# Kernel tuning notes

Hardware: AMD Instinct MI355X
Metric: run time of the kernel (lower is better)

Reference implementation:

```python
import jax, jax.numpy as jnp
import numpy as np

B, CIN, H, W = 1024, 1, 200, 32   # batch, in_channels, feat_nums, embed_dim
COUT = 16                          # out_channels
K = 3                              # con_kernel (height)
TOPK = 50                          # min(feat_nums, topk)
# ZeroPad2d padding for kernel (K,1): width (0,0), height (K//2 + K - 2*(K//2) - 1, K//2)
PAD_TOP = K // 2 + K - 2 * (K // 2) - 1
PAD_BOT = K // 2


def setup_inputs() -> dict:
    key = jax.random.key(0)
    k1, k2, k3 = jax.random.split(key, 3)
    x = jax.random.normal(k1, (B, CIN, H, W), dtype=jnp.float32)
    conv_w = jax.random.normal(k2, (COUT, CIN, K, 1), dtype=jnp.float32) * 0.1
    conv_b = jax.random.normal(k3, (COUT,), dtype=jnp.float32) * 0.1
    return {"x": x, "conv_w": conv_w, "conv_b": conv_b}


def reference(x, conv_w, conv_b):
    # 'same' conv along H only (kernel width is 1), stride 1
    y = jax.lax.conv_general_dilated(
        x, conv_w,
        window_strides=(1, 1),
        padding=((PAD_TOP, PAD_BOT), (0, 0)),
        dimension_numbers=("NCHW", "OIHW", "NCHW"),
    )
    y = jnp.tanh(y + conv_b[None, :, None, None])  # [B, COUT, H, W]
    # top-k along H (dim 2), values sorted descending (matches torch.topk)
    yt = jnp.swapaxes(y, 2, 3)                      # [B, COUT, W, H]
    vals, _ = jax.lax.top_k(yt, TOPK)               # [B, COUT, W, TOPK]
    return jnp.swapaxes(vals, 2, 3)                 # [B, COUT, TOPK, W]
```

## Files before the change

### kernel.cpp

```cpp
#include <hip/hip_runtime.h>
#include <math.h>

#define B_     1024
#define H_     200
#define W_     32
#define COUT_  16
#define TOPK_  50

#define XST 17
#define OST 17

typedef _Float16 h2 __attribute__((ext_vector_type(2)));
union HU { h2 h; int i; };

constexpr unsigned long long lane_mask(int J, int K) {
    unsigned long long m = 0;
    for (int l = 0; l < 64; ++l) {
        bool a = (l & J) != 0;
        bool b = (K < 64) && ((l & K) != 0);
        if (a != b) m |= (1ull << l);
    }
    return m;
}

#define X_1(o,v)  "v_mov_b32_dpp " o ", " v " quad_perm:[1,0,3,2] row_mask:0xf bank_mask:0xf\n\t"
#define X_2(o,v)  "v_mov_b32_dpp " o ", " v " quad_perm:[2,3,0,1] row_mask:0xf bank_mask:0xf\n\t"
#define X_8(o,v)  "v_mov_b32_dpp " o ", " v " row_ror:8 row_mask:0xf bank_mask:0xf\n\t"
#define X_4(o,v)  "ds_swizzle_b32 " o ", " v " offset:0x101F\n\t"
#define X_16(o,v) "ds_swizzle_b32 " o ", " v " offset:0x401F\n\t"
#define X_32(o,v) "ds_bpermute_b32 " o ", %[pa], " v "\n\t"
#define PRE_1  "s_nop 4\n\t"
#define PRE_2  "s_nop 4\n\t"
#define PRE_8  "s_nop 4\n\t"
#define PRE_4  ""
#define PRE_16 ""
#define PRE_32 ""
#define WAIT_1  ""
#define WAIT_2  ""
#define WAIT_8  ""
#define WAIT_4  "s_waitcnt lgkmcnt(0)\n\t"
#define WAIT_16 "s_waitcnt lgkmcnt(0)\n\t"
#define WAIT_32 "s_waitcnt lgkmcnt(0)\n\t"

#define S6(J, K) { constexpr unsigned long long M = lane_mask(J, K); \
  int o0,o1,o2,o3,o4,o5; \
  asm volatile( PRE_##J \
    X_##J("%[o0]","%[x0]") X_##J("%[o1]","%[x1]") X_##J("%[o2]","%[x2]") \
    X_##J("%[o3]","%[x3]") X_##J("%[o4]","%[x4]") X_##J("%[o5]","%[x5]") \
    WAIT_##J \
    "s_mov_b64 exec, %[m]\n\t" \
    "v_pk_max_f16 %[x0], %[x0], %[o0]\n\t" \
    "v_pk_max_f16 %[x1], %[x1], %[o1]\n\t" \
    "v_pk_min_f16 %[x2], %[x2], %[o2]\n\t" \
    "v_pk_min_f16 %[x3], %[x3], %[o3]\n\t" \
    "v_pk_max_f16 %[x4], %[x4], %[o4]\n\t" \
    "v_pk_max_f16 %[x5], %[x5], %[o5]\n\t" \
    "s_not_b64 exec, exec\n\t" \
    "v_pk_min_f16 %[x0], %[x0], %[o0]\n\t" \
    "v_pk_min_f16 %[x1], %[x1], %[o1]\n\t" \
    "v_pk_max_f16 %[x2], %[x2], %[o2]\n\t" \
    "v_pk_max_f16 %[x3], %[x3], %[o3]\n\t" \
    "v_pk_min_f16 %[x4], %[x4], %[o4]\n\t" \
    "v_pk_min_f16 %[x5], %[x5], %[o5]\n\t" \
    "s_mov_b64 exec, -1\n\t" \
    : [x0]"+v"(v0a),[x1]"+v"(v0b),[x2]"+v"(v1a),[x3]"+v"(v1b),[x4]"+v"(v2a),[x5]"+v"(v2b), \
      [o0]"=&v"(o0),[o1]"=&v"(o1),[o2]"=&v"(o2),[o3]"=&v"(o3),[o4]"=&v"(o4),[o5]"=&v"(o5) \
    : [m]"s"(M), [pa]"v"(paddr)); }

#define P2N(J, K, A, B) { constexpr unsigned long long M = lane_mask(J, K); \
  int oA,oB; \
  asm volatile( PRE_##J \
    X_##J("%[xA2]","%[xA]") X_##J("%[xB2]","%[xB]") \
    WAIT_##J \
    "s_mov_b64 exec, %[m]\n\t" \
    "v_pk_min_f16 %[xA], %[xA], %[xA2]\n\t" \
    "v_pk_min_f16 %[xB], %[xB], %[xB2]\n\t" \
    "s_not_b64 exec, exec\n\t" \
    "v_pk_max_f16 %[xA], %[xA], %[xA2]\n\t" \
    "v_pk_max_f16 %[xB], %[xB], %[xB2]\n\t" \
    "s_mov_b64 exec, -1\n\t" \
    : [xA]"+v"(A),[xB]"+v"(B),[xA2]"=&v"(oA),[xB2]"=&v"(oB) \
    : [m]"s"(M), [pa]"v"(paddr)); }

#define M4(J) { constexpr unsigned long long M = lane_mask(J, 64); \
  int o0,o1,o2,o3; \
  asm volatile( PRE_##J \
    X_##J("%[o0]","%[x0]") X_##J("%[o1]","%[x1]") X_##J("%[o2]","%[x2]") X_##J("%[o3]","%[x3]") \
    WAIT_##J \
    "s_mov_b64 exec, %[m]\n\t" \
    "v_pk_max_f16 %[x0], %[x0], %[o0]\n\t" \
    "v_pk_max_f16 %[x1], %[x1], %[o1]\n\t" \
    "v_pk_min_f16 %[x2], %[x2], %[o2]\n\t" \
    "v_pk_min_f16 %[x3], %[x3], %[o3]\n\t" \
    "s_not_b64 exec, exec\n\t" \
    "v_pk_min_f16 %[x0], %[x0], %[o0]\n\t" \
    "v_pk_min_f16 %[x1], %[x1], %[o1]\n\t" \
    "v_pk_max_f16 %[x2], %[x2], %[o2]\n\t" \
    "v_pk_max_f16 %[x3], %[x3], %[o3]\n\t" \
    "s_mov_b64 exec, -1\n\t" \
    : [x0]"+v"(m1a),[x1]"+v"(m1b),[x2]"+v"(m2a),[x3]"+v"(m2b), \
      [o0]"=&v"(o0),[o1]"=&v"(o1),[o2]"=&v"(o2),[o3]"=&v"(o3) \
    : [m]"s"(M), [pa]"v"(paddr)); }

__device__ __forceinline__ int pkmax(int a, int b) {
    int r;
    asm("v_pk_max_f16 %0, %1, %2" : "=v"(r) : "v"(a), "v"(b));
    return r;
}

__device__ __forceinline__ float fast_tanh(float s) {
    float e = __expf(2.0f * s);
    return fmaf(-2.0f, __builtin_amdgcn_rcpf(e + 1.0f), 1.0f);
}

__global__ __launch_bounds__(256, 8) void cnn_topk_kernel(
    const float* __restrict__ x,
    const float* __restrict__ cw,
    const float* __restrict__ cb,
    float* __restrict__ out)
{
    __shared__ float xs[(H_ + 2) * XST];
    __shared__ int   obuf[TOPK_ * OST];

    const int b   = blockIdx.x >> 1;
    const int wh  = blockIdx.x & 1;
    const int tid = threadIdx.x;
    const float* xb = x + (size_t)b * (H_ * W_) + wh * 16;

    for (int i = tid; i < H_ * 4; i += 256) {
        int h = i >> 2, q = (i & 3) * 4;
        float4 v = *reinterpret_cast<const float4*>(xb + h * W_ + q);
        float* d = &xs[(h + 1) * XST + q];
        d[0] = v.x; d[1] = v.y; d[2] = v.z; d[3] = v.w;
    }
    if (tid < 16) {
        xs[tid] = 0.0f;
        xs[(H_ + 1) * XST + tid] = 0.0f;
    }
    __syncthreads();

    const int wave = tid >> 6;
    const int lane = tid & 63;
    const int paddr = (lane ^ 32) << 2;

    const int SENT = (int)0xFC00FC00;
    const int h3 = (192 + lane < H_) ? (192 + lane) : (H_ - 1);

#pragma unroll 1
    for (int cp = 0; cp < 8; ++cp) {
        const int coA = 2 * cp, coB = 2 * cp + 1;
        const float w0A = cw[coA * 3], w1A = cw[coA * 3 + 1], w2A = cw[coA * 3 + 2], bA = cb[coA];
        const float w0B = cw[coB * 3], w1B = cw[coB * 3 + 1], w2B = cw[coB * 3 + 2], bB = cb[coB];

#pragma unroll
        for (int wp = 0; wp < 2; ++wp) {
            const int wA = wave * 4 + wp * 2;
            const int wB = wA + 1;

            int v0a, v1a, v2a, v3a, v0b, v1b, v2b, v3b;
#define MAKE_V(VR, HROW, WC)                                                 \
            {   const int hh = (HROW);                                       \
                float xm = xs[ hh      * XST + (WC)];                        \
                float xc = xs[(hh + 1) * XST + (WC)];                        \
                float xp = xs[(hh + 2) * XST + (WC)];                        \
                float sA = fmaf(w2A, xp, fmaf(w1A, xc, fmaf(w0A, xm, bA)));  \
                float sB = fmaf(w2B, xp, fmaf(w1B, xc, fmaf(w0B, xm, bB)));  \
                VR = __builtin_bit_cast(int, __builtin_amdgcn_cvt_pkrtz(sA, sB)); }
            MAKE_V(v0a, lane, wA)       MAKE_V(v0b, lane, wB)
            MAKE_V(v1a, 64 + lane, wA)  MAKE_V(v1b, 64 + lane, wB)
            MAKE_V(v2a, 128 + lane, wA) MAKE_V(v2b, 128 + lane, wB)
            MAKE_V(v3a, h3, wA)         MAKE_V(v3b, h3, wB)
#undef MAKE_V
            v3a = (lane < 8) ? v3a : SENT;
            v3b = (lane < 8) ? v3b : SENT;

            S6(1, 2)
            S6(2, 4)  S6(1, 4)
            S6(4, 8)  S6(2, 8)  S6(1, 8)
            S6(8, 16) S6(4, 16) S6(2, 16) S6(1, 16)
            S6(16,32) S6(8, 32) S6(4, 32) S6(2, 32) S6(1, 32)
            S6(32,64) S6(16,64) S6(8, 64) S6(4, 64) S6(2, 64) S6(1, 64)

            P2N(1, 2, v3a, v3b)
            P2N(2, 4, v3a, v3b)  P2N(1, 4, v3a, v3b)
            P2N(4, 8, v3a, v3b)  P2N(2, 8, v3a, v3b)  P2N(1, 8, v3a, v3b)

            int m1a = pkmax(v0a, v1a), m1b = pkmax(v0b, v1b);
            int m2a = pkmax(v2a, v3a), m2b = pkmax(v2b, v3b);
            M4(32) M4(16) M4(8) M4(4) M4(2) M4(1)
            int ta = pkmax(m1a, m2a), tb = pkmax(m1b, m2b);
            P2N(32, 64, ta, tb) P2N(16, 64, ta, tb) P2N(8, 64, ta, tb)
            P2N(4, 64, ta, tb)  P2N(2, 64, ta, tb)  P2N(1, 64, ta, tb)

            if (lane < TOPK_) {
                obuf[lane * OST + wA] = ta;
                obuf[lane * OST + wB] = tb;
            }
        }
        __syncthreads();

#pragma unroll
        for (int j = 0; j < 4; ++j) {
            int idx = tid + j * 256;
            if (idx < 800) {
                int k = idx >> 4, w2 = idx & 15;
                HU u; u.i = obuf[k * OST + w2];
                size_t o0 = (((size_t)b * COUT_ + coA) * TOPK_ + k) * W_ + wh * 16 + w2;
                out[o0]                        = fast_tanh((float)u.h.x);
                out[o0 + (size_t)TOPK_ * W_]   = fast_tanh((float)u.h.y);
            }
        }
        __syncthreads();
    }
}

extern "C" void kernel_launch(void* const* d_in, const int* in_sizes, int n_in,
                              void* d_out, int out_size, void* d_ws, size_t ws_size,
                              hipStream_t stream) {
    const float* x  = (const float*)d_in[0];
    const float* cw = (const float*)d_in[1];
    const float* cb = (const float*)d_in[2];
    float* out = (float*)d_out;

    cnn_topk_kernel<<<dim3(B_ * 2), dim3(256), 0, stream>>>(x, cw, cb, out);
}
```

Baseline: 250.5 us.

## Restructure bitonic top-k so each 16-lane group handles one column

Each 16-lane group now owns one output column and holds 13 packed half2 values per lane, where before a full wave sorted 200 rows of one column pair. Most bitonic stages become in-register compare-exchanges, and lane exchanges only use DPP and ds_swizzle within 16 lanes, so the ds_bpermute and xor-16 swizzle are gone. This removes cross-row LDS permute traffic and the serial loop over column pairs per wave. The cost is more live registers and a more intricate merge network, with some risk to correctness.

Measured after the change: 230.0 us. 8.2% less time.

```diff
diff --git a/kernel.cpp b/kernel.cpp
--- a/kernel.cpp
+++ b/kernel.cpp
@@ -13,100 +13,146 @@
 typedef _Float16 h2 __attribute__((ext_vector_type(2)));
 union HU { h2 h; int i; };
 
-constexpr unsigned long long lane_mask(int J, int K) {
+
+constexpr unsigned long long lmask(int d, int Kb) {
     unsigned long long m = 0;
     for (int l = 0; l < 64; ++l) {
-        bool a = (l & J) != 0;
-        bool b = (K < 64) && ((l & K) != 0);
+        int ln = l & 15;
+        bool a = (ln & d) != 0;
+        bool b = Kb && ((ln & Kb) != 0);
         if (a != b) m |= (1ull << l);
     }
     return m;
 }
 
-#define X_1(o,v)  "v_mov_b32_dpp " o ", " v " quad_perm:[1,0,3,2] row_mask:0xf bank_mask:0xf\n\t"
-#define X_2(o,v)  "v_mov_b32_dpp " o ", " v " quad_perm:[2,3,0,1] row_mask:0xf bank_mask:0xf\n\t"
-#define X_8(o,v)  "v_mov_b32_dpp " o ", " v " row_ror:8 row_mask:0xf bank_mask:0xf\n\t"
-#define X_4(o,v)  "ds_swizzle_b32 " o ", " v " offset:0x101F\n\t"
-#define X_16(o,v) "ds_swizzle_b32 " o ", " v " offset:0x401F\n\t"
-#define X_32(o,v) "ds_bpermute_b32 " o ", %[pa], " v "\n\t"
-#define PRE_1  "s_nop 4\n\t"
-#define PRE_2  "s_nop 4\n\t"
-#define PRE_8  "s_nop 4\n\t"
-#define PRE_4  ""
-#define PRE_16 ""
-#define PRE_32 ""
-#define WAIT_1  ""
-#define WAIT_2  ""
-#define WAIT_8  ""
-#define WAIT_4  "s_waitcnt lgkmcnt(0)\n\t"
-#define WAIT_16 "s_waitcnt lgkmcnt(0)\n\t"
-#define WAIT_32 "s_waitcnt lgkmcnt(0)\n\t"
-
-#define S6(J, K) { constexpr unsigned long long M = lane_mask(J, K); \
-  int o0,o1,o2,o3,o4,o5; \
-  asm volatile( PRE_##J \
-    X_##J("%[o0]","%[x0]") X_##J("%[o1]","%[x1]") X_##J("%[o2]","%[x2]") \
-    X_##J("%[o3]","%[x3]") X_##J("%[o4]","%[x4]") X_##J("%[o5]","%[x5]") \
-    WAIT_##J \
+#define XOP_1(o,v) "v_mov_b32_dpp " o ", " v " quad_perm:[1,0,3,2] row_mask:0xf bank_mask:0xf\n\t"
+#define XOP_2(o,v) "v_mov_b32_dpp " o ", " v " quad_perm:[2,3,0,1] row_mask:0xf bank_mask:0xf\n\t"
+#define XOP_8(o,v) "v_mov_b32_dpp " o ", " v " row_ror:8 row_mask:0xf bank_mask:0xf\n\t"
+#define XOP_4(o,v) "ds_swizzle_b32 " o ", " v " offset:0x101F\n\t"
+#define PRE_1 "s_nop 4\n\t"
+#define PRE_2 "s_nop 4\n\t"
+#define PRE_8 "s_nop 4\n\t"
+#define PRE_4 ""
+#define WAIT_1 ""
+#define WAIT_2 ""
+#define WAIT_8 ""
+#define WAIT_4 "s_waitcnt lgkmcnt(0)\n\t"
+
+#define P1_MX "v_pk_max_f16 "
+#define P1_MN "v_pk_min_f16 "
+#define P2_MX "v_pk_min_f16 "
+#define P2_MN "v_pk_max_f16 "
+#define OP_(ph,t,x,o) ph##_##t x ", " x ", " o "\n\t"
+
+#define SRT12(d, Kb, t0,t1,t2,t3,t4,t5,t6,t7,t8,t9,tA,tB) { \
+  constexpr unsigned long long M_ = lmask(d, Kb); \
+  int o0,o1,o2,o3,o4,o5,o6,o7,o8,o9,oA,oB; \
+  asm volatile( PRE_##d \
+    XOP_##d("%[o0]","%[x0]") XOP_##d("%[o1]","%[x1]") \
+    XOP_##d("%[o2]","%[x2]") XOP_##d("%[o3]","%[x3]") \
+    XOP_##d("%[o4]","%[x4]") XOP_##d("%[o5]","%[x5]") \
+    XOP_##d("%[o6]","%[x6]") XOP_##d("%[o7]","%[x7]") \
+    XOP_##d("%[o8]","%[x8]") XOP_##d("%[o9]","%[x9]") \
+    XOP_##d("%[oA]","%[xA]") XOP_##d("%[oB]","%[xB]") \
+    WAIT_##d \
+    "s_mov_b64 exec, %[m]\n\t" \
+    OP_(P1,t0,"%[x0]","%[o0]") OP_(P1,t1,"%[x1]","%[o1]") \
+    OP_(P1,t2,"%[x2]","%[o2]") OP_(P1,t3,"%[x3]","%[o3]") \
+    OP_(P1,t4,"%[x4]","%[o4]") OP_(P1,t5,"%[x5]","%[o5]") \
+    OP_(P1,t6,"%[x6]","%[o6]") OP_(P1,t7,"%[x7]","%[o7]") \
+    OP_(P1,t8,"%[x8]","%[o8]") OP_(P1,t9,"%[x9]","%[o9]") \
+    OP_(P1,tA,"%[xA]","%[oA]") OP_(P1,tB,"%[xB]","%[oB]") \
+    "s_not_b64 exec, exec\n\t" \
+    OP_(P2,t0,"%[x0]","%[o0]") OP_(P2,t1,"%[x1]","%[o1]") \
+    OP_(P2,t2,"%[x2]","%[o2]") OP_(P2,t3,"%[x3]","%[o3]") \
+    OP_(P2,t4,"%[x4]","%[o4]") OP_(P2,t5,"%[x5]","%[o5]") \
+    OP_(P2,t6,"%[x6]","%[o6]") OP_(P2,t7,"%[x7]","%[o7]") \
+    OP_(P2,t8,"%[x8]","%[o8]") OP_(P2,t9,"%[x9]","%[o9]") \
+    OP_(P2,tA,"%[xA]","%[oA]") OP_(P2,tB,"%[xB]","%[oB]") \
+    "s_mov_b64 exec, -1\n\t" \
+    : [x0]"+v"(a0),[x1]"+v"(a1),[x2]"+v"(a2),[x3]"+v"(a3), \
+      [x4]"+v"(b0),[x5]"+v"(b1),[x6]"+v"(b2),[x7]"+v"(b3), \
+      [x8]"+v"(e0),[x9]"+v"(e1),[xA]"+v"(e2),[xB]"+v"(e3), \
+      [o0]"=&v"(o0),[o1]"=&v"(o1),[o2]"=&v"(o2),[o3]"=&v"(o3), \
+      [o4]"=&v"(o4),[o5]"=&v"(o5),[o6]"=&v"(o6),[o7]"=&v"(o7), \
+      [o8]"=&v"(o8),[o9]"=&v"(o9),[oA]"=&v"(oA),[oB]"=&v"(oB) \
+    : [m]"s"(M_)); }
+
+#define SRT_A(d,Kb) SRT12(d,Kb, MX,MX,MX,MX, MN,MN,MN,MN, MX,MX,MX,MX)
+#define SRT_B(d)    SRT12(d,0,  MX,MN,MX,MN, MN,MX,MN,MX, MX,MN,MX,MN)
+#define SRT_C(d)    SRT12(d,0,  MX,MX,MN,MN, MN,MN,MX,MX, MX,MX,MN,MN)
+
+#define C3(d, Kb) { constexpr unsigned long long M_ = lmask(d, Kb); int oF; \
+  asm volatile( PRE_##d XOP_##d("%[oF]","%[xF]") WAIT_##d \
+    "s_mov_b64 exec, %[m]\n\t" \
+    "v_pk_min_f16 %[xF], %[xF], %[oF]\n\t" \
+    "s_not_b64 exec, exec\n\t" \
+    "v_pk_max_f16 %[xF], %[xF], %[oF]\n\t" \
+    "s_mov_b64 exec, -1\n\t" \
+    : [xF]"+v"(f0), [oF]"=&v"(oF) : [m]"s"(M_)); }
+
+#define MRG8(d) { constexpr unsigned long long M_ = lmask(d, 0); \
+  int o0,o1,o2,o3,o4,o5,o6,o7; \
+  asm volatile( PRE_##d \
+    XOP_##d("%[o0]","%[x0]") XOP_##d("%[o1]","%[x1]") \
+    XOP_##d("%[o2]","%[x2]") XOP_##d("%[o3]","%[x3]") \
+    XOP_##d("%[o4]","%[x4]") XOP_##d("%[o5]","%[x5]") \
+    XOP_##d("%[o6]","%[x6]") XOP_##d("%[o7]","%[x7]") \
+    WAIT_##d \
     "s_mov_b64 exec, %[m]\n\t" \
     "v_pk_max_f16 %[x0], %[x0], %[o0]\n\t" \
     "v_pk_max_f16 %[x1], %[x1], %[o1]\n\t" \
+    "v_pk_max_f16 %[x2], %[x2], %[o2]\n\t" \
+    "v_pk_max_f16 %[x3], %[x3], %[o3]\n\t" \
+    "v_pk_min_f16 %[x4], %[x4], %[o4]\n\t" \
+    "v_pk_min_f16 %[x5], %[x5], %[o5]\n\t" \
+    "v_pk_min_f16 %[x6], %[x6], %[o6]\n\t" \
+    "v_pk_min_f16 %[x7], %[x7], %[o7]\n\t" \
+    "s_not_b64 exec, exec\n\t" \
+    "v_pk_min_f16 %[x0], %[x0], %[o0]\n\t" \
+    "v_pk_min_f16 %[x1], %[x1], %[o1]\n\t" \
     "v_pk_min_f16 %[x2], %[x2], %[o2]\n\t" \
     "v_pk_min_f16 %[x3], %[x3], %[o3]\n\t" \
     "v_pk_max_f16 %[x4], %[x4], %[o4]\n\t" \
     "v_pk_max_f16 %[x5], %[x5], %[o5]\n\t" \
-    "s_not_b64 exec, exec\n\t" \
+    "v_pk_max_f16 %[x6], %[x6], %[o6]\n\t" \
+    "v_pk_max_f16 %[x7], %[x7], %[o7]\n\t" \
+    "s_mov_b64 exec, -1\n\t" \
+    : [x0]"+v"(g0),[x1]"+v"(g1),[x2]"+v"(g2),[x3]"+v"(g3), \
+      [x4]"+v"(e0),[x5]"+v"(e1),[x6]"+v"(e2),[x7]"+v"(e3), \
+      [o0]"=&v"(o0),[o1]"=&v"(o1),[o2]"=&v"(o2),[o3]"=&v"(o3), \
+      [o4]"=&v"(o4),[o5]"=&v"(o5),[o6]"=&v"(o6),[o7]"=&v"(o7) \
+    : [m]"s"(M_)); }
+
+#define FIN4(d) { constexpr unsigned long long M_ = lmask(d, 0); \
+  int o0,o1,o2,o3; \
+  asm volatile( PRE_##d \
+    XOP_##d("%[o0]","%[x0]") XOP_##d("%[o1]","%[x1]") \
+    XOP_##d("%[o2]","%[x2]") XOP_##d("%[o3]","%[x3]") \
+    WAIT_##d \
+    "s_mov_b64 exec, %[m]\n\t" \
     "v_pk_min_f16 %[x0], %[x0], %[o0]\n\t" \
     "v_pk_min_f16 %[x1], %[x1], %[o1]\n\t" \
+    "v_pk_min_f16 %[x2], %[x2], %[o2]\n\t" \
+    "v_pk_min_f16 %[x3], %[x3], %[o3]\n\t" \
+    "s_not_b64 exec, exec\n\t" \
+    "v_pk_max_f16 %[x0], %[x0], %[o0]\n\t" \
+    "v_pk_max_f16 %[x1], %[x1], %[o1]\n\t" \
     "v_pk_max_f16 %[x2], %[x2], %[o2]\n\t" \
     "v_pk_max_f16 %[x3], %[x3], %[o3]\n\t" \
-    "v_pk_min_f16 %[x4], %[x4], %[o4]\n\t" \
-    "v_pk_min_f16 %[x5], %[x5], %[o5]\n\t" \
-    "s_mov_b64 exec, -1\n\t" \
-    : [x0]"+v"(v0a),[x1]"+v"(v0b),[x2]"+v"(v1a),[x3]"+v"(v1b),[x4]"+v"(v2a),[x5]"+v"(v2b), \
-      [o0]"=&v"(o0),[o1]"=&v"(o1),[o2]"=&v"(o2),[o3]"=&v"(o3),[o4]"=&v"(o4),[o5]"=&v"(o5) \
-    : [m]"s"(M), [pa]"v"(paddr)); }
-
-#define P2N(J, K, A, B) { constexpr unsigned long long M = lane_mask(J, K); \
-  int oA,oB; \
-  asm volatile( PRE_##J \
-    X_##J("%[xA2]","%[xA]") X_##J("%[xB2]","%[xB]") \
-    WAIT_##J \
-    "s_mov_b64 exec, %[m]\n\t" \
-    "v_pk_min_f16 %[xA], %[xA], %[xA2]\n\t" \
-    "v_pk_min_f16 %[xB], %[xB], %[xB2]\n\t" \
-    "s_not_b64 exec, exec\n\t" \
-    "v_pk_max_f16 %[xA], %[xA], %[xA2]\n\t" \
-    "v_pk_max_f16 %[xB], %[xB], %[xB2]\n\t" \
-    "s_mov_b64 exec, -1\n\t" \
-    : [xA]"+v"(A),[xB]"+v"(B),[xA2]"=&v"(oA),[xB2]"=&v"(oB) \
-    : [m]"s"(M), [pa]"v"(paddr)); }
-
-#define M4(J) { constexpr unsigned long long M = lane_mask(J, 64); \
-  int o0,o1,o2,o3; \
-  asm volatile( PRE_##J \
-    X_##J("%[o0]","%[x0]") X_##J("%[o1]","%[x1]") X_##J("%[o2]","%[x2]") X_##J("%[o3]","%[x3]") \
-    WAIT_##J \
-    "s_mov_b64 exec, %[m]\n\t" \
-    "v_pk_max_f16 %[x0], %[x0], %[o0]\n\t" \
-    "v_pk_max_f16 %[x1], %[x1], %[o1]\n\t" \
-    "v_pk_min_f16 %[x2], %[x2], %[o2]\n\t" \
-    "v_pk_min_f16 %[x3], %[x3], %[o3]\n\t" \
-    "s_not_b64 exec, exec\n\t" \
-    "v_pk_min_f16 %[x0], %[x0], %[o0]\n\t" \
-    "v_pk_min_f16 %[x1], %[x1], %[o1]\n\t" \
-    "v_pk_max_f16 %[x2], %[x2], %[o2]\n\t" \
-    "v_pk_max_f16 %[x3], %[x3], %[o3]\n\t" \
-    "s_mov_b64 exec, -1\n\t" \
-    : [x0]"+v"(m1a),[x1]"+v"(m1b),[x2]"+v"(m2a),[x3]"+v"(m2b), \
+    "s_mov_b64 exec, -1\n\t" \
+    : [x0]"+v"(g0),[x1]"+v"(g1),[x2]"+v"(g2),[x3]"+v"(g3), \
       [o0]"=&v"(o0),[o1]"=&v"(o1),[o2]"=&v"(o2),[o3]"=&v"(o3) \
-    : [m]"s"(M), [pa]"v"(paddr)); }
-
-__device__ __forceinline__ int pkmax(int a, int b) {
-    int r;
-    asm("v_pk_max_f16 %0, %1, %2" : "=v"(r) : "v"(a), "v"(b));
-    return r;
-}
+    : [m]"s"(M_)); }
+
+__device__ __forceinline__ int pkmx(int a, int b) {
+    int r; asm("v_pk_max_f16 %0, %1, %2" : "=v"(r) : "v"(a), "v"(b)); return r;
+}
+__device__ __forceinline__ int pkmn(int a, int b) {
+    int r; asm("v_pk_min_f16 %0, %1, %2" : "=v"(r) : "v"(a), "v"(b)); return r;
+}
+#define RCE(A,B,FLIP) { int mn_ = pkmn(A,B), mx_ = pkmx(A,B); \
+  if (FLIP) { A = mx_; B = mn_; } else { A = mn_; B = mx_; } }
 
 __device__ __forceinline__ float fast_tanh(float s) {
     float e = __expf(2.0f * s);
@@ -141,10 +187,15 @@
 
     const int wave = tid >> 6;
     const int lane = tid & 63;
-    const int paddr = (lane ^ 32) << 2;
+    const int ln   = lane & 15;
+    const int col  = wave * 4 + (lane >> 4);
 
     const int SENT = (int)0xFC00FC00;
-    const int h3 = (192 + lane < H_) ? (192 + lane) : (H_ - 1);
+    const bool tail_ok = (ln < 8);
+    const int h3t = (192 + ln < H_) ? (192 + ln) : (H_ - 1);
+    const float* xsf = &xs[ln * XST + col];
+    const float* xst = &xs[h3t * XST + col];
+    int* obase = &obuf[ln * OST + col];
 
 #pragma unroll 1
     for (int cp = 0; cp < 8; ++cp) {
@@ -152,51 +203,48 @@
         const float w0A = cw[coA * 3], w1A = cw[coA * 3 + 1], w2A = cw[coA * 3 + 2], bA = cb[coA];
         const float w0B = cw[coB * 3], w1B = cw[coB * 3 + 1], w2B = cw[coB * 3 + 2], bB = cb[coB];
 
-#pragma unroll
-        for (int wp = 0; wp < 2; ++wp) {
-            const int wA = wave * 4 + wp * 2;
-            const int wB = wA + 1;
-
-            int v0a, v1a, v2a, v3a, v0b, v1b, v2b, v3b;
-#define MAKE_V(VR, HROW, WC)                                                 \
-            {   const int hh = (HROW);                                       \
-                float xm = xs[ hh      * XST + (WC)];                        \
-                float xc = xs[(hh + 1) * XST + (WC)];                        \
-                float xp = xs[(hh + 2) * XST + (WC)];                        \
-                float sA = fmaf(w2A, xp, fmaf(w1A, xc, fmaf(w0A, xm, bA)));  \
-                float sB = fmaf(w2B, xp, fmaf(w1B, xc, fmaf(w0B, xm, bB)));  \
-                VR = __builtin_bit_cast(int, __builtin_amdgcn_cvt_pkrtz(sA, sB)); }
-            MAKE_V(v0a, lane, wA)       MAKE_V(v0b, lane, wB)
-            MAKE_V(v1a, 64 + lane, wA)  MAKE_V(v1b, 64 + lane, wB)
-            MAKE_V(v2a, 128 + lane, wA) MAKE_V(v2b, 128 + lane, wB)
-            MAKE_V(v3a, h3, wA)         MAKE_V(v3b, h3, wB)
-#undef MAKE_V
-            v3a = (lane < 8) ? v3a : SENT;
-            v3b = (lane < 8) ? v3b : SENT;
-
-            S6(1, 2)
-            S6(2, 4)  S6(1, 4)
-            S6(4, 8)  S6(2, 8)  S6(1, 8)
-            S6(8, 16) S6(4, 16) S6(2, 16) S6(1, 16)
-            S6(16,32) S6(8, 32) S6(4, 32) S6(2, 32) S6(1, 32)
-            S6(32,64) S6(16,64) S6(8, 64) S6(4, 64) S6(2, 64) S6(1, 64)
-
-            P2N(1, 2, v3a, v3b)
-            P2N(2, 4, v3a, v3b)  P2N(1, 4, v3a, v3b)
-            P2N(4, 8, v3a, v3b)  P2N(2, 8, v3a, v3b)  P2N(1, 8, v3a, v3b)
-
-            int m1a = pkmax(v0a, v1a), m1b = pkmax(v0b, v1b);
-            int m2a = pkmax(v2a, v3a), m2b = pkmax(v2b, v3b);
-            M4(32) M4(16) M4(8) M4(4) M4(2) M4(1)
-            int ta = pkmax(m1a, m2a), tb = pkmax(m1b, m2b);
-            P2N(32, 64, ta, tb) P2N(16, 64, ta, tb) P2N(8, 64, ta, tb)
-            P2N(4, 64, ta, tb)  P2N(2, 64, ta, tb)  P2N(1, 64, ta, tb)
-
-            if (lane < TOPK_) {
-                obuf[lane * OST + wA] = ta;
-                obuf[lane * OST + wB] = tb;
-            }
-        }
+        int a0,a1,a2,a3,b0,b1,b2,b3,e0,e1,e2,e3,f0;
+#define CONV1(VR, CO) { \
+        float xm = xsf[(CO)*XST], xc = xsf[((CO)+1)*XST], xp = xsf[((CO)+2)*XST]; \
+        float sA = fmaf(w2A, xp, fmaf(w1A, xc, fmaf(w0A, xm, bA))); \
+        float sB = fmaf(w2B, xp, fmaf(w1B, xc, fmaf(w0B, xm, bB))); \
+        VR = __builtin_bit_cast(int, __builtin_amdgcn_cvt_pkrtz(sA, sB)); }
+        CONV1(a0, 0)   CONV1(a1, 16)  CONV1(a2, 32)  CONV1(a3, 48)
+        CONV1(b0, 64)  CONV1(b1, 80)  CONV1(b2, 96)  CONV1(b3, 112)
+        CONV1(e0, 128) CONV1(e1, 144) CONV1(e2, 160) CONV1(e3, 176)
+        { float xm = xst[0], xc = xst[XST], xp = xst[2*XST];
+          float sA = fmaf(w2A, xp, fmaf(w1A, xc, fmaf(w0A, xm, bA)));
+          float sB = fmaf(w2B, xp, fmaf(w1B, xc, fmaf(w0B, xm, bB)));
+          int vt = __builtin_bit_cast(int, __builtin_amdgcn_cvt_pkrtz(sA, sB));
+          f0 = tail_ok ? vt : SENT; }
+#undef CONV1
+
+        SRT_A(1, 2)
+        SRT_A(2, 4) SRT_A(1, 4)
+        SRT_A(4, 8) SRT_A(2, 8) SRT_A(1, 8)
+        SRT_B(8) SRT_B(4) SRT_B(2) SRT_B(1)
+        RCE(a0,a1,0) RCE(a2,a3,1) RCE(b0,b1,1) RCE(b2,b3,0) RCE(e0,e1,0) RCE(e2,e3,1)
+        SRT_C(8) SRT_C(4) SRT_C(2) SRT_C(1)
+        RCE(a0,a2,0) RCE(a1,a3,0) RCE(b0,b2,1) RCE(b1,b3,1) RCE(e0,e2,0) RCE(e1,e3,0)
+        RCE(a0,a1,0) RCE(a2,a3,0) RCE(b0,b1,1) RCE(b2,b3,1) RCE(e0,e1,0) RCE(e2,e3,0)
+        SRT_A(8, 0) SRT_A(4, 0) SRT_A(2, 0) SRT_A(1, 0)
+
+        C3(1, 2) C3(2, 4) C3(1, 4) C3(4, 0) C3(2, 0) C3(1, 0)
+
+        int g0 = pkmx(a0, b0), g1 = pkmx(a1, b1), g2 = pkmx(a2, b2), g3 = pkmx(a3, b3);
+        e0 = pkmx(e0, f0);
+        RCE(g0,g2,0) RCE(g1,g3,0) RCE(e0,e2,1) RCE(e1,e3,1)
+        RCE(g0,g1,0) RCE(g2,g3,0) RCE(e0,e1,1) RCE(e2,e3,1)
+        MRG8(8) MRG8(4) MRG8(2) MRG8(1)
+        g0 = pkmx(g0, e0); g1 = pkmx(g1, e1); g2 = pkmx(g2, e2); g3 = pkmx(g3, e3);
+        RCE(g0,g2,1) RCE(g1,g3,1)
+        RCE(g0,g1,1) RCE(g2,g3,1)
+        FIN4(8) FIN4(4) FIN4(2) FIN4(1)
+
+        obase[0]            = g0;
+        obase[16 * OST]     = g1;
+        obase[32 * OST]     = g2;
+        if (ln < 2) obase[48 * OST] = g3;
         __syncthreads();
 
 #pragma unroll
```
